# Kernel optimization log

Hardware: AMD Instinct MI355X
Metric: run time of the kernel (lower is better)

Reference implementation:

```python
import jax, jax.numpy as jnp
import numpy as np

B, P, N = 32, 64, 8192
EPS_CASE = 0.0001  # hard-coded threshold in fc_of_edge's tf.where


def setup_inputs() -> dict:
    key = jax.random.key(0)
    k1, k2 = jax.random.split(key)
    points = jax.random.normal(k1, (B, P, 2), dtype=jnp.float32)
    # phi grid comes from fc_tensor[0, 0, :] in the original ctor; use angles in [0, 2*pi)
    phi = jax.random.uniform(k2, (N,), dtype=jnp.float32) * (2.0 * np.pi)
    return {"points": points, "phi": phi}


def reference(points, phi):
    # q(phi) = [cos(phi), sin(phi) - 1], shape [2, N]
    q = jnp.stack([jnp.cos(phi), jnp.sin(phi) - 1.0])
    cross = jnp.array([[0.0, -1.0], [1.0, 0.0]], dtype=points.dtype)
    q_cross = cross @ q                                   # [2, N]
    scale = 1.0 / jnp.abs(q[0] ** 2 + q[1] ** 2)          # [N], real

    # vectorize the python edge loop: edge k is (points[:, k-1], points[:, k])
    p1 = points                                           # [B, P, 2]
    p0 = jnp.roll(points, 1, axis=1)                      # [B, P, 2]
    d = p1 - p0

    dot = lambda a, b: jnp.einsum('bpi,in->bpn', a, b)    # [B, P, N]
    dp0q = dot(p0, q)
    dp1q = dot(p1, q)
    ddq = dot(d, q)
    ddqc = dot(d, q_cross)

    j = jnp.complex64(1j)
    f_p0 = -jnp.exp(j * dp0q)                             # c = 0 in fc_of_phi
    f_p1 = -jnp.exp(j * dp1q)

    mask = jnp.abs(ddq) >= EPS_CASE
    ddq_safe = jnp.where(mask, ddq, 1.0)                  # avoid div-by-~0 in unused branch
    case1 = scale * ddqc * (f_p1 - f_p0) / ddq_safe
    case2 = scale * ddqc * (-j) * jnp.exp(j * dp0q)
    res = jnp.where(mask, case1, case2)                   # [B, P, N] complex64

    sum_res = jnp.sum(res, axis=1)                        # [B, N]
    # original: concat(real, imag) along axis=1 of [B, 1, N] -> [B, 2, N]
    return jnp.stack([jnp.real(sum_res), jnp.imag(sum_res)], axis=1)
```

## Files before the change

### kernel.cpp

```cpp
#include <hip/hip_runtime.h>
#include <math.h>

#define BATCH 32
#define PTS   64
#define NPHI  8192

__device__ __forceinline__ void sincosf_f64(float xf, float* s, float* c) {
    const double PIO2_HI = 1.57079632679489661923e+00;
    const double PIO2_LO = 6.12323399573676603587e-17;

    const float kf = __builtin_rintf(__fmul_rn(xf, 0.63661977236758138243f));
    const int   qi = (int)kf;
    const double kd = (double)kf;
    const double x  = (double)xf;

    double r = __builtin_fma(-kd, PIO2_HI, x);
    r = __builtin_fma(-kd, PIO2_LO, r);
    const double r2 = r * r;

    double ps = -2.50507602534068634195e-08;
    ps = __builtin_fma(ps, r2,  2.75573137070700676789e-06);
    ps = __builtin_fma(ps, r2, -1.98412698298579493134e-04);
    ps = __builtin_fma(ps, r2,  8.33333333332248946124e-03);
    ps = __builtin_fma(ps, r2, -1.66666666666666324348e-01);
    const double sinr = __builtin_fma(r * r2, ps, r);

    double pc =  2.08757232129817482790e-09;
    pc = __builtin_fma(pc, r2, -2.75573143513906633035e-07);
    pc = __builtin_fma(pc, r2,  2.48015872894767294178e-05);
    pc = __builtin_fma(pc, r2, -1.38888888888741095749e-03);
    pc = __builtin_fma(pc, r2,  4.16666666666666019037e-02);
    const double cosr = __builtin_fma(r2 * r2, pc, __builtin_fma(-0.5, r2, 1.0));

    const float sf = (float)sinr, cf = (float)cosr;
    const bool sw = (qi & 1);
    const float ss = sw ? cf : sf;
    const float cc = sw ? sf : cf;
    *s = (qi & 2)       ? -ss : ss;
    *c = ((qi + 1) & 2) ? -cc : cc;
}

__device__ __forceinline__ void sincosf_f32(float x, float* s, float* c) {
    const float C1 = 1.5707969665527344f;
    const float C2 = -6.3975783777e-7f;

    const float kf = __builtin_rintf(x * 0.63661977236758f);
    const int   qi = (int)kf;
    const float r1 = __builtin_fmaf(-kf, C1, x);
    const float r  = __builtin_fmaf(-kf, C2, r1);
    const float r2 = r * r;

    float ps = __builtin_fmaf(2.75573137e-06f, r2, -1.98412698e-04f);
    ps = __builtin_fmaf(ps, r2,  8.33333333e-03f);
    ps = __builtin_fmaf(ps, r2, -1.66666667e-01f);
    const float sr = __builtin_fmaf(r * r2, ps, r);

    float pc = __builtin_fmaf(-2.75573144e-07f, r2, 2.48015873e-05f);
    pc = __builtin_fmaf(pc, r2, -1.38888889e-03f);
    pc = __builtin_fmaf(pc, r2,  4.16666667e-02f);
    const float u  = __builtin_fmaf(r2 * r2, pc, -(0.5f * r2));
    const float cr = 1.0f + u;

    const bool sw = (qi & 1);
    const float ss = sw ? cr : sr;
    const float cc = sw ? sr : cr;
    *s = (qi & 2)       ? -ss : ss;
    *c = ((qi + 1) & 2) ? -cc : cc;
}

__global__ __launch_bounds__(256, 8) void scatter_polygon_kernel(
    const float* __restrict__ points,
    const float* __restrict__ phi,
    float* __restrict__ out)
{
    __shared__ float spts[2 * PTS];

    const int b = blockIdx.y;
    const int tid = threadIdx.x;
    const int h = tid & 1;
    const int n = blockIdx.x * 128 + (tid >> 1);

    if (tid < 2 * PTS) {
        spts[tid] = points[b * 2 * PTS + tid];
    }
    __syncthreads();

    const float ph = phi[n];
    float sph, cph;
    sincosf_f64(ph, &sph, &cph);
    const float q0  = cph;
    const float q1  = __fsub_rn(sph, 1.0f);
    const float nq1 = -q1;
    const float scale =
        1.0f / fabsf(__fadd_rn(__fmul_rn(q0, q0), __fmul_rn(q1, q1)));

    const int p0i = h ? (PTS / 2 - 1) : (PTS - 1);
    float xp = spts[2 * p0i];
    float yp = spts[2 * p0i + 1];
    const float dp_prev = __fadd_rn(__fmul_rn(xp, q0), __fmul_rn(yp, q1));
    float s0, c0;
    sincosf_f32(dp_prev, &s0, &c0);

    float accR = 0.0f, accI = 0.0f;
    const int pbase = h * (PTS / 2);

    #pragma unroll 4
    for (int i = 0; i < PTS / 2; ++i) {
        const int p = pbase + i;
        const float x = spts[2 * p];
        const float y = spts[2 * p + 1];
        const float dp_cur = __fadd_rn(__fmul_rn(x, q0), __fmul_rn(y, q1));
        float s1, c1;
        sincosf_f32(dp_cur, &s1, &c1);

        const float dx = __fsub_rn(x, xp);
        const float dy = __fsub_rn(y, yp);
        const float ddq  = __fadd_rn(__fmul_rn(dx, q0),  __fmul_rn(dy, q1));
        const float ddqc = __fadd_rn(__fmul_rn(dx, nq1), __fmul_rn(dy, q0));

        const bool  m1  = (fabsf(ddq) >= 1e-4f);
        const float inv = __builtin_amdgcn_rcpf(ddq);
        const float dR = __fsub_rn(c0, c1);
        const float dI = __fsub_rn(s0, s1);
        const float gR = m1 ? (dR * inv) : s0;
        const float gI = m1 ? (dI * inv) : (-c0);
        accR = __builtin_fmaf(ddqc, gR, accR);
        accI = __builtin_fmaf(ddqc, gI, accI);

        xp = x; yp = y; c0 = c1; s0 = s1;
    }

    const float totR = scale * (accR + __shfl_xor(accR, 1));
    const float totI = scale * (accI + __shfl_xor(accI, 1));

    if (h == 0) {
        out[(size_t)b * 2 * NPHI + n]        = totR;
        out[(size_t)b * 2 * NPHI + NPHI + n] = totI;
    }
}

extern "C" void kernel_launch(void* const* d_in, const int* in_sizes, int n_in,
                              void* d_out, int out_size, void* d_ws, size_t ws_size,
                              hipStream_t stream) {
    const float* points = (const float*)d_in[0];
    const float* phi    = (const float*)d_in[1];
    float* out          = (float*)d_out;

    dim3 grid(NPHI / 128, BATCH);
    scatter_polygon_kernel<<<grid, 256, 0, stream>>>(points, phi, out);
}
```

Before: 74.79 us.

## Precompute phi table in separate kernel and pack sincos polynomials into vec2 FMAs

A new pre-kernel evaluates the double-precision sincos of phi once per angle and writes q0, q1 and scale to a workspace table. Before, every batch block recomputed this, 32 times redundantly. The per-point sincos polynomial now evaluates its sine and cosine branches together as two-wide float vectors, so the compiler can emit packed FMA (v_pk_fma_f32), and the accumulators are packed the same way. Points load as float2 and the unroll factor rises to 8. The cost is an extra kernel launch and a workspace round trip, plus possible register pressure under the 8-wave launch bound.

```diff
diff --git a/kernel.cpp b/kernel.cpp
--- a/kernel.cpp
+++ b/kernel.cpp
@@ -4,6 +4,8 @@
 #define BATCH 32
 #define PTS   64
 #define NPHI  8192
+
+typedef float v2f __attribute__((ext_vector_type(2)));
 
 __device__ __forceinline__ void sincosf_f64(float xf, float* s, float* c) {
     const double PIO2_HI = 1.57079632679489661923e+00;
@@ -40,7 +42,19 @@
     *c = ((qi + 1) & 2) ? -cc : cc;
 }
 
-__device__ __forceinline__ void sincosf_f32(float x, float* s, float* c) {
+__global__ __launch_bounds__(256) void phi_table_kernel(
+    const float* __restrict__ phi, float4* __restrict__ qtab) {
+    const int n = blockIdx.x * 256 + threadIdx.x;
+    float sph, cph;
+    sincosf_f64(phi[n], &sph, &cph);
+    const float q0 = cph;
+    const float q1 = __fsub_rn(sph, 1.0f);
+    const float scale =
+        1.0f / fabsf(__fadd_rn(__fmul_rn(q0, q0), __fmul_rn(q1, q1)));
+    qtab[n] = make_float4(q0, q1, scale, 0.0f);
+}
+
+__device__ __forceinline__ v2f sincos2_f32(float x) {
     const float C1 = 1.5707969665527344f;
     const float C2 = -6.3975783777e-7f;
 
@@ -50,88 +64,77 @@
     const float r  = __builtin_fmaf(-kf, C2, r1);
     const float r2 = r * r;
 
-    float ps = __builtin_fmaf(2.75573137e-06f, r2, -1.98412698e-04f);
-    ps = __builtin_fmaf(ps, r2,  8.33333333e-03f);
-    ps = __builtin_fmaf(ps, r2, -1.66666667e-01f);
-    const float sr = __builtin_fmaf(r * r2, ps, r);
-
-    float pc = __builtin_fmaf(-2.75573144e-07f, r2, 2.48015873e-05f);
-    pc = __builtin_fmaf(pc, r2, -1.38888889e-03f);
-    pc = __builtin_fmaf(pc, r2,  4.16666667e-02f);
-    const float u  = __builtin_fmaf(r2 * r2, pc, -(0.5f * r2));
-    const float cr = 1.0f + u;
+    const v2f rr = (v2f){r2, r2};
+    v2f p = (v2f){2.75573137e-06f, -2.75573144e-07f};
+    p = __builtin_elementwise_fma(p, rr, (v2f){-1.98412698e-04f, 2.48015873e-05f});
+    p = __builtin_elementwise_fma(p, rr, (v2f){ 8.33333333e-03f, -1.38888889e-03f});
+    p = __builtin_elementwise_fma(p, rr, (v2f){-1.66666667e-01f, 4.16666667e-02f});
+    const v2f a = (v2f){r * r2, r2 * r2};
+    const v2f bt = (v2f){r, __builtin_fmaf(-0.5f, r2, 1.0f)};
+    const v2f sc = __builtin_elementwise_fma(a, p, bt);
 
     const bool sw = (qi & 1);
-    const float ss = sw ? cr : sr;
-    const float cc = sw ? sr : cr;
-    *s = (qi & 2)       ? -ss : ss;
-    *c = ((qi + 1) & 2) ? -cc : cc;
+    float ss = sw ? sc.y : sc.x;
+    float cc = sw ? sc.x : sc.y;
+    ss = (qi & 2)       ? -ss : ss;
+    cc = ((qi + 1) & 2) ? -cc : cc;
+    return (v2f){ss, cc};
 }
 
 __global__ __launch_bounds__(256, 8) void scatter_polygon_kernel(
     const float* __restrict__ points,
-    const float* __restrict__ phi,
+    const float4* __restrict__ qtab,
     float* __restrict__ out)
 {
-    __shared__ float spts[2 * PTS];
+    __shared__ float2 spts[PTS];
 
     const int b = blockIdx.y;
     const int tid = threadIdx.x;
     const int h = tid & 1;
     const int n = blockIdx.x * 128 + (tid >> 1);
 
-    if (tid < 2 * PTS) {
-        spts[tid] = points[b * 2 * PTS + tid];
+    if (tid < PTS) {
+        spts[tid] = reinterpret_cast<const float2*>(points)[b * PTS + tid];
     }
     __syncthreads();
 
-    const float ph = phi[n];
-    float sph, cph;
-    sincosf_f64(ph, &sph, &cph);
-    const float q0  = cph;
-    const float q1  = __fsub_rn(sph, 1.0f);
+    const float4 qv = qtab[n];
+    const float q0 = qv.x, q1 = qv.y, scale = qv.z;
     const float nq1 = -q1;
-    const float scale =
-        1.0f / fabsf(__fadd_rn(__fmul_rn(q0, q0), __fmul_rn(q1, q1)));
 
     const int p0i = h ? (PTS / 2 - 1) : (PTS - 1);
-    float xp = spts[2 * p0i];
-    float yp = spts[2 * p0i + 1];
+    float2 pv = spts[p0i];
+    float xp = pv.x, yp = pv.y;
     const float dp_prev = __fadd_rn(__fmul_rn(xp, q0), __fmul_rn(yp, q1));
-    float s0, c0;
-    sincosf_f32(dp_prev, &s0, &c0);
+    v2f sc0 = sincos2_f32(dp_prev);
 
-    float accR = 0.0f, accI = 0.0f;
+    v2f acc = (v2f){0.0f, 0.0f};
     const int pbase = h * (PTS / 2);
 
-    #pragma unroll 4
+    #pragma unroll 8
     for (int i = 0; i < PTS / 2; ++i) {
-        const int p = pbase + i;
-        const float x = spts[2 * p];
-        const float y = spts[2 * p + 1];
-        const float dp_cur = __fadd_rn(__fmul_rn(x, q0), __fmul_rn(y, q1));
-        float s1, c1;
-        sincosf_f32(dp_cur, &s1, &c1);
+        const float2 v = spts[pbase + i];
+        const float dp = __fadd_rn(__fmul_rn(v.x, q0), __fmul_rn(v.y, q1));
+        const v2f sc1 = sincos2_f32(dp);
 
-        const float dx = __fsub_rn(x, xp);
-        const float dy = __fsub_rn(y, yp);
+        const float dx = __fsub_rn(v.x, xp);
+        const float dy = __fsub_rn(v.y, yp);
         const float ddq  = __fadd_rn(__fmul_rn(dx, q0),  __fmul_rn(dy, q1));
         const float ddqc = __fadd_rn(__fmul_rn(dx, nq1), __fmul_rn(dy, q0));
 
         const bool  m1  = (fabsf(ddq) >= 1e-4f);
         const float inv = __builtin_amdgcn_rcpf(ddq);
-        const float dR = __fsub_rn(c0, c1);
-        const float dI = __fsub_rn(s0, s1);
-        const float gR = m1 ? (dR * inv) : s0;
-        const float gI = m1 ? (dI * inv) : (-c0);
-        accR = __builtin_fmaf(ddqc, gR, accR);
-        accI = __builtin_fmaf(ddqc, gI, accI);
+        const v2f d = sc0 - sc1;
+        v2f g;
+        g.x = m1 ? (d.x * inv) : (-sc0.y);
+        g.y = m1 ? (d.y * inv) : ( sc0.x);
+        acc = __builtin_elementwise_fma((v2f){ddqc, ddqc}, g, acc);
 
-        xp = x; yp = y; c0 = c1; s0 = s1;
+        xp = v.x; yp = v.y; sc0 = sc1;
     }
 
-    const float totR = scale * (accR + __shfl_xor(accR, 1));
-    const float totI = scale * (accI + __shfl_xor(accI, 1));
+    const float totR = scale * (acc.y + __shfl_xor(acc.y, 1));
+    const float totI = scale * (acc.x + __shfl_xor(acc.x, 1));
 
     if (h == 0) {
         out[(size_t)b * 2 * NPHI + n]        = totR;
@@ -145,7 +148,10 @@
     const float* points = (const float*)d_in[0];
     const float* phi    = (const float*)d_in[1];
     float* out          = (float*)d_out;
+    float4* qtab        = (float4*)d_ws;
+
+    phi_table_kernel<<<NPHI / 256, 256, 0, stream>>>(phi, qtab);
 
     dim3 grid(NPHI / 128, BATCH);
-    scatter_polygon_kernel<<<grid, 256, 0, stream>>>(points, phi, out);
+    scatter_polygon_kernel<<<grid, 256, 0, stream>>>(points, qtab, out);
 }
```

New measurement: 75.84 us. About the same (+1.4%).

## Use one thread per phi and read polygon points directly from global memory

Applied to the files above, without the earlier changes.

Each thread now handles one phi value over all 64 edges, instead of two threads splitting the edges and combining their partial sums with a shuffle. The shared-memory staging and the block barrier are gone: points are read through wave-uniform global loads, which can become scalar loads. This halves the thread count and removes the duplicated f64 sincos per phi, but lengthens each thread's serial loop, leaves half as many waves to hide latency, and relaxes the launch bounds occupancy hint.

```diff
diff --git a/kernel.cpp b/kernel.cpp
--- a/kernel.cpp
+++ b/kernel.cpp
@@ -68,22 +68,14 @@
     *c = ((qi + 1) & 2) ? -cc : cc;
 }
 
-__global__ __launch_bounds__(256, 8) void scatter_polygon_kernel(
+__global__ __launch_bounds__(256, 4) void scatter_polygon_kernel(
     const float* __restrict__ points,
     const float* __restrict__ phi,
     float* __restrict__ out)
 {
-    __shared__ float spts[2 * PTS];
-
     const int b = blockIdx.y;
-    const int tid = threadIdx.x;
-    const int h = tid & 1;
-    const int n = blockIdx.x * 128 + (tid >> 1);
-
-    if (tid < 2 * PTS) {
-        spts[tid] = points[b * 2 * PTS + tid];
-    }
-    __syncthreads();
+    const int n = blockIdx.x * 256 + threadIdx.x;
+    const float* __restrict__ pb = points + b * 2 * PTS;
 
     const float ph = phi[n];
     float sph, cph;
@@ -94,24 +86,21 @@
     const float scale =
         1.0f / fabsf(__fadd_rn(__fmul_rn(q0, q0), __fmul_rn(q1, q1)));
 
-    const int p0i = h ? (PTS / 2 - 1) : (PTS - 1);
-    float xp = spts[2 * p0i];
-    float yp = spts[2 * p0i + 1];
+    float xp = pb[2 * (PTS - 1)];
+    float yp = pb[2 * (PTS - 1) + 1];
     const float dp_prev = __fadd_rn(__fmul_rn(xp, q0), __fmul_rn(yp, q1));
     float s0, c0;
     sincosf_f32(dp_prev, &s0, &c0);
 
     float accR = 0.0f, accI = 0.0f;
-    const int pbase = h * (PTS / 2);
 
-    #pragma unroll 4
-    for (int i = 0; i < PTS / 2; ++i) {
-        const int p = pbase + i;
-        const float x = spts[2 * p];
-        const float y = spts[2 * p + 1];
-        const float dp_cur = __fadd_rn(__fmul_rn(x, q0), __fmul_rn(y, q1));
+    #pragma unroll 8
+    for (int p = 0; p < PTS; ++p) {
+        const float x = pb[2 * p];
+        const float y = pb[2 * p + 1];
+        const float dp = __fadd_rn(__fmul_rn(x, q0), __fmul_rn(y, q1));
         float s1, c1;
-        sincosf_f32(dp_cur, &s1, &c1);
+        sincosf_f32(dp, &s1, &c1);
 
         const float dx = __fsub_rn(x, xp);
         const float dy = __fsub_rn(y, yp);
@@ -130,13 +119,8 @@
         xp = x; yp = y; c0 = c1; s0 = s1;
     }
 
-    const float totR = scale * (accR + __shfl_xor(accR, 1));
-    const float totI = scale * (accI + __shfl_xor(accI, 1));
-
-    if (h == 0) {
-        out[(size_t)b * 2 * NPHI + n]        = totR;
-        out[(size_t)b * 2 * NPHI + NPHI + n] = totI;
-    }
+    out[(size_t)b * 2 * NPHI + n]        = scale * accR;
+    out[(size_t)b * 2 * NPHI + NPHI + n] = scale * accI;
 }
 
 extern "C" void kernel_launch(void* const* d_in, const int* in_sizes, int n_in,
@@ -146,6 +130,6 @@
     const float* phi    = (const float*)d_in[1];
     float* out          = (float*)d_out;
 
-    dim3 grid(NPHI / 128, BATCH);
+    dim3 grid(NPHI / 256, BATCH);
     scatter_polygon_kernel<<<grid, 256, 0, stream>>>(points, phi, out);
 }
```

Result: no change. 75.76 us (+1.3%).
